# Optimization experiments

Hardware: AMD Instinct MI355X
Metric: run time of the kernel (lower is better)

## Reference

```python
import jax, jax.numpy as jnp
import numpy as np

B, H, W, D, C = 1, 32, 32, 32, 512
NH, P = 8, 8
HD = C // NH          # head dim = 64
N = P ** 3            # tokens per window = 512
HID = 4 * C           # mlp hidden = 2048
EPS = 1e-5            # torch LayerNorm default


def setup_inputs() -> dict:
    key = jax.random.key(0)
    ks = jax.random.split(key, 8)
    init = lambda k, shape, fan: jax.random.normal(k, shape, jnp.float32) / np.sqrt(fan).astype(np.float32)
    return {
        "x": jax.random.normal(ks[0], (B, H, W, D, C), jnp.float32),
        "q_ms": jax.random.normal(ks[1], (B, NH, N, HD), jnp.float32),
        "norm1_w": jnp.ones((C,), jnp.float32),
        "norm1_b": jnp.zeros((C,), jnp.float32),
        "kv_w": init(ks[2], (C, 2 * C), C),
        "kv_b": jnp.zeros((2 * C,), jnp.float32),
        "proj_w": init(ks[3], (C, C), C),
        "proj_b": jnp.zeros((C,), jnp.float32),
        "norm2_w": jnp.ones((C,), jnp.float32),
        "norm2_b": jnp.zeros((C,), jnp.float32),
        "fc1_w": init(ks[4], (C, HID), C),
        "fc1_b": jnp.zeros((HID,), jnp.float32),
        "fc2_w": init(ks[5], (HID, C), HID),
        "fc2_b": jnp.zeros((C,), jnp.float32),
    }


def layernorm(x, w, b):
    m = jnp.mean(x, axis=-1, keepdims=True)
    v = jnp.mean(jnp.square(x - m), axis=-1, keepdims=True)
    return (x - m) * jax.lax.rsqrt(v + EPS) * w + b


def reference(x, q_ms, norm1_w, norm1_b, kv_w, kv_b, proj_w, proj_b,
              norm2_w, norm2_b, fc1_w, fc1_b, fc2_w, fc2_b):
    shortcut = x
    xn = layernorm(x, norm1_w, norm1_b)
    # get_patches: (B,H,W,D,C) -> (B*nw, N, C), windows in (nh,nw,nd) order
    xw = xn.reshape(B, H // P, P, W // P, P, D // P, P, C)
    xw = xw.transpose(0, 1, 3, 5, 2, 4, 6, 7).reshape(-1, N, C)
    Bw = xw.shape[0]  # B * num_windows = 64
    # global attention: kv from window tokens, shared multi-scale query q_ms
    kv = (xw @ kv_w + kv_b).reshape(Bw, N, 2, NH, HD).transpose(2, 0, 3, 1, 4)
    k, v = kv[0], kv[1]  # (Bw, NH, N, HD)
    scale = HD ** -0.5
    q = jnp.tile(q_ms, (Bw // B, 1, 1, 1)) * scale  # replicate query across windows
    attn = jax.nn.softmax(jnp.einsum('bhqd,bhkd->bhqk', q, k), axis=-1)
    o = jnp.einsum('bhqk,bhkd->bhqd', attn, v)
    o = o.transpose(0, 2, 1, 3).reshape(Bw, N, C)
    o = o @ proj_w + proj_b
    # get_image: (B*nw, N, C) -> (B,H,W,D,C)
    xi = o.reshape(B, H // P, W // P, D // P, P, P, P, C)
    xi = xi.transpose(0, 1, 4, 2, 5, 3, 6, 7).reshape(B, H, W, D, C)
    x1 = shortcut + xi
    h = layernorm(x1, norm2_w, norm2_b)
    h = jax.nn.gelu(h @ fc1_w + fc1_b, approximate=False) @ fc2_w + fc2_b
    return x1 + h
```

## Files before the change

### kernel.cpp

```cpp
#include <hip/hip_runtime.h>

typedef unsigned short u16;
typedef __attribute__((ext_vector_type(8))) short bfrag;
typedef __attribute__((ext_vector_type(4))) float ffrag;

#define LN_EPS 1e-5f

#define GLOAD16(g, l)                                                          \
    __builtin_amdgcn_global_load_lds(                                          \
        (const __attribute__((address_space(1))) void*)(g),                    \
        (__attribute__((address_space(3))) void*)(l), 16, 0, 0)

__device__ __forceinline__ u16 f2bf(float f) {
    unsigned u = __builtin_bit_cast(unsigned, f);
    u += 0x7fffu + ((u >> 16) & 1u);
    return (u16)(u >> 16);
}

__device__ __forceinline__ int win_to_img(int tok) {
    int win = tok >> 9, n = tok & 511;
    int wh = win >> 4, ww = (win >> 2) & 3, wd = win & 3;
    int ph = n >> 6, pw = (n >> 3) & 7, pd = n & 7;
    return ((wh * 8 + ph) * 32 + (ww * 8 + pw)) * 32 + (wd * 8 + pd);
}

__global__ __launch_bounds__(256) void k_ln(const float* __restrict__ x,
                                            const float* __restrict__ w,
                                            const float* __restrict__ b,
                                            u16* __restrict__ out, int windowed) {
    int wave = threadIdx.x >> 6, lane = threadIdx.x & 63;
    int tok = blockIdx.x * 4 + wave;
    int src = windowed ? win_to_img(tok) : tok;
    const float* xr = x + (size_t)src * 512;
    float v[8];
#pragma unroll
    for (int i = 0; i < 2; i++) {
        float4 f = *(const float4*)(xr + i * 256 + lane * 4);
        v[i * 4 + 0] = f.x; v[i * 4 + 1] = f.y; v[i * 4 + 2] = f.z; v[i * 4 + 3] = f.w;
    }
    float s = 0.f;
#pragma unroll
    for (int i = 0; i < 8; i++) s += v[i];
#pragma unroll
    for (int m = 1; m < 64; m <<= 1) s += __shfl_xor(s, m);
    float mean = s * (1.0f / 512.0f);
    float vs = 0.f;
#pragma unroll
    for (int i = 0; i < 8; i++) { float d = v[i] - mean; vs += d * d; }
#pragma unroll
    for (int m = 1; m < 64; m <<= 1) vs += __shfl_xor(vs, m);
    float rstd = rsqrtf(vs * (1.0f / 512.0f) + LN_EPS);
    u16* orow = out + (size_t)tok * 512;
#pragma unroll
    for (int i = 0; i < 2; i++) {
        int c0 = i * 256 + lane * 4;
        ushort4 o;
        o.x = f2bf((v[i * 4 + 0] - mean) * rstd * w[c0 + 0] + b[c0 + 0]);
        o.y = f2bf((v[i * 4 + 1] - mean) * rstd * w[c0 + 1] + b[c0 + 1]);
        o.z = f2bf((v[i * 4 + 2] - mean) * rstd * w[c0 + 2] + b[c0 + 2]);
        o.w = f2bf((v[i * 4 + 3] - mean) * rstd * w[c0 + 3] + b[c0 + 3]);
        *(ushort4*)(orow + c0) = o;
    }
}

__global__ __launch_bounds__(256) void k_prep(const float* __restrict__ kv_w,
                                              const float* __restrict__ proj_w,
                                              const float* __restrict__ fc1_w,
                                              const float* __restrict__ fc2_w,
                                              const float* __restrict__ q,
                                              u16* __restrict__ kv_wt,
                                              u16* __restrict__ proj_wt,
                                              u16* __restrict__ fc1_wt,
                                              u16* __restrict__ fc2_wt,
                                              u16* __restrict__ qbf) {
    int i = blockIdx.x * 256 + threadIdx.x;
    if (i < 524288) {
        int n = i >> 9, k = i & 511;
        kv_wt[i] = f2bf(kv_w[k * 1024 + n]);
    } else if (i < 786432) {
        int j = i - 524288, n = j >> 9, k = j & 511;
        proj_wt[j] = f2bf(proj_w[k * 512 + n]);
    } else if (i < 1835008) {
        int j = i - 786432, n = j >> 9, k = j & 511;
        fc1_wt[j] = f2bf(fc1_w[k * 2048 + n]);
    } else if (i < 2883584) {
        int j = i - 1835008, n = j >> 11, k = j & 2047;
        fc2_wt[j] = f2bf(fc2_w[k * 512 + n]);
    } else {
        int j = i - 2883584;
        qbf[j] = f2bf(q[j] * 0.125f);
    }
}

template <int EPI>
__global__ __launch_bounds__(256, 4) void k_gemm128(const u16* __restrict__ A,
                                                    const u16* __restrict__ Bt,
                                                    const float* __restrict__ bias,
                                                    void* __restrict__ Cout, int K, int Nn,
                                                    const float* __restrict__ resid,
                                                    void* __restrict__ Cout2) {
    __shared__ u16 As0[4096], Bs0[4096], As1[4096], Bs1[4096];
    int tid = threadIdx.x;
    int wave = tid >> 6, lane = tid & 63;
    int wr = wave >> 1, wc = wave & 1;

    int gx = Nn >> 7;
    int nwg = gridDim.x;
    int wg = blockIdx.x;
    int wgs = (wg & 7) * (nwg >> 3) + (wg >> 3);
    int bn = wgs % gx, bm = wgs / gx;

    int rt = wave * 32 + (lane >> 2);
    int sxo = ((lane & 3) ^ ((rt ^ (rt >> 2)) & 3)) * 8;
    const u16* Ag = A + (size_t)(bm * 128 + rt) * K + sxo;
    const u16* Bg = Bt + (size_t)(bn * 128 + rt) * K + sxo;

    int fr = lane & 15, g = lane >> 4;
    int pco = (g ^ ((fr ^ (fr >> 2)) & 3)) * 8;

    ffrag acc[4][4] = {};

#define STAGE(AS, BS, k0)                                                      \
    {                                                                          \
        GLOAD16(Ag + (k0), AS + wave * 1024);                                  \
        GLOAD16(Ag + (k0) + 16 * K, AS + wave * 1024 + 512);                   \
        GLOAD16(Bg + (k0), BS + wave * 1024);                                  \
        GLOAD16(Bg + (k0) + 16 * K, BS + wave * 1024 + 512);                   \
    }
#define COMPUTE(AS, BS)                                                        \
    {                                                                          \
        bfrag a[4], b[4];                                                      \
        _Pragma("unroll") for (int m = 0; m < 4; m++)                          \
            a[m] = *(const bfrag*)(AS + (wr * 64 + m * 16 + fr) * 32 + pco);   \
        _Pragma("unroll") for (int n = 0; n < 4; n++)                          \
            b[n] = *(const bfrag*)(BS + (wc * 64 + n * 16 + fr) * 32 + pco);   \
        _Pragma("unroll") for (int m = 0; m < 4; m++)                          \
            _Pragma("unroll") for (int n = 0; n < 4; n++)                      \
                acc[m][n] = __builtin_amdgcn_mfma_f32_16x16x32_bf16(           \
                    a[m], b[n], acc[m][n], 0, 0, 0);                           \
    }

    int nt = K >> 5;
    STAGE(As0, Bs0, 0);
    __syncthreads();
    int t = 0;
    for (; t + 2 < nt; t += 2) {
        STAGE(As1, Bs1, (t + 1) * 32);
        COMPUTE(As0, Bs0);
        __syncthreads();
        STAGE(As0, Bs0, (t + 2) * 32);
        COMPUTE(As1, Bs1);
        __syncthreads();
    }
    STAGE(As1, Bs1, (nt - 1) * 32);
    COMPUTE(As0, Bs0);
    __syncthreads();
    COMPUTE(As1, Bs1);
#undef STAGE
#undef COMPUTE

    int gcolb = bn * 128 + wc * 64;
    int grb = bm * 128 + wr * 64;

    if constexpr (EPI == 0 || EPI == 2) {
        __syncthreads();
        u16* ep = (wave == 0) ? As0 : (wave == 1) ? Bs0 : (wave == 2) ? As1 : Bs1;
        int h = (gcolb >> 6) & 7;
        bool isK = (EPI == 2) || (gcolb < 512);
#pragma unroll
        for (int m = 0; m < 4; m++)
#pragma unroll
            for (int n = 0; n < 4; n++) {
                float bv = bias[gcolb + n * 16 + fr];
#pragma unroll
                for (int r = 0; r < 4; r++) {
                    int wq = m * 16 + g * 4 + r;
                    int wcc = n * 16 + fr;
                    float val = acc[m][n][r] + bv;
                    if constexpr (EPI == 2) {
                        float xx = val;
                        float inner = fmaf(0.044715f * xx * xx, xx, xx);
                        float e = __expf(-1.5957691216f * inner);
                        val = xx * __builtin_amdgcn_rcpf(1.0f + e);
                    }
                    if (isK)
                        ep[wq * 64 + (wcc ^ ((wq & 7) << 3))] = f2bf(val);
                    else
                        ep[wcc * 64 + (wq ^ ((wcc & 7) << 3))] = f2bf(val);
                }
            }
#pragma unroll
        for (int rd = 0; rd < 8; rd++) {
            int row = rd * 8 + (lane >> 3);
            int ch = (lane & 7) ^ (row & 7);
            int4 v = *(const int4*)(ep + row * 64 + ch * 8);
            if constexpr (EPI == 2) {
                int grow = grb + row;
                *(int4*)(&((u16*)Cout)[(size_t)grow * Nn + gcolb + (lane & 7) * 8]) = v;
            } else {
                if (isK) {
                    int tok = grb + row;
                    int win = tok >> 9, key = tok & 511;
                    *(int4*)(&((u16*)Cout)[(((size_t)(win * 8 + h)) * 512 + key) * 64 + (lane & 7) * 8]) = v;
                } else {
                    int win = grb >> 9, key0 = grb & 511;
                    *(int4*)(&((u16*)Cout2)[(((size_t)(win * 8 + h)) * 64 + row) * 512 + key0 + (lane & 7) * 8]) = v;
                }
            }
        }
    } else {
#pragma unroll
        for (int m = 0; m < 4; m++)
#pragma unroll
            for (int n = 0; n < 4; n++) {
                int col = gcolb + n * 16 + fr;
                float bv = bias[col];
#pragma unroll
                for (int r = 0; r < 4; r++) {
                    int row = grb + m * 16 + g * 4 + r;
                    float val = acc[m][n][r] + bv;
                    if constexpr (EPI == 1) {
                        int ri = win_to_img(row);
                        size_t o = (size_t)ri * 512 + col;
                        ((float*)Cout)[o] = val + resid[o];
                    } else {
                        size_t o = (size_t)row * 512 + col;
                        ((float*)Cout)[o] = val + resid[o];
                    }
                }
            }
    }
}

__global__ __launch_bounds__(256, 4) void k_attn(const u16* __restrict__ qb,
                                                 const u16* __restrict__ kb,
                                                 const u16* __restrict__ vtb,
                                                 u16* __restrict__ o) {
    __shared__ u16 K0[4096], K1[4096], V0[4096], V1[4096];
    __shared__ u16 Ps[4096];
    int bid = blockIdx.x;
    int wg = (bid & 7) * 512 + (bid >> 3);
    int qc = wg & 7;
    int pair = wg >> 3;
    int hh = pair & 7, win = pair >> 3;
    int wave = threadIdx.x >> 6, lane = threadIdx.x & 63;
    const u16* kbw = kb + ((size_t)(win * 8 + hh)) * 512 * 64;
    const u16* vtw = vtb + ((size_t)(win * 8 + hh)) * 64 * 512;

    const u16* qrow = qb + ((size_t)hh * 512 + qc * 64 + (wave << 4) + (lane & 15)) * 64 + (lane >> 4) * 8;
    bfrag aq0 = *(const bfrag*)(qrow);
    bfrag aq1 = *(const bfrag*)(qrow + 32);

    ffrag acc[4] = {};
    float m_run[4], l_run[4];
#pragma unroll
    for (int r = 0; r < 4; r++) { m_run[r] = -1e30f; l_run[r] = 0.0f; }

    int srow = lane >> 3;
    int sxo = ((lane & 7) ^ srow) * 8;
    int fr = lane & 15;
    int fkc = lane >> 4;
    int kx0 = (fkc ^ (fr & 7)) * 8;
    int kx1 = ((fkc + 4) ^ (fr & 7)) * 8;
    int arow = (wave << 4) + fr;
    int pswz = (arow & 7) << 3;

#define STAGE_KV(KS, VS, kc)                                                   \
    {                                                                          \
        GLOAD16(kbw + (size_t)((kc) * 64 + wave * 8 + srow) * 64 + sxo,        \
                KS + wave * 512);                                              \
        GLOAD16(kbw + (size_t)((kc) * 64 + 32 + wave * 8 + srow) * 64 + sxo,   \
                KS + 2048 + wave * 512);                                       \
        GLOAD16(vtw + (size_t)(wave * 8 + srow) * 512 + (kc) * 64 + sxo,       \
                VS + wave * 512);                                              \
        GLOAD16(vtw + (size_t)(32 + wave * 8 + srow) * 512 + (kc) * 64 + sxo,  \
                VS + 2048 + wave * 512);                                       \
    }
#define ATT_COMPUTE(KS, VS)                                                    \
    {                                                                          \
        ffrag s[4] = {};                                                       \
        _Pragma("unroll") for (int j = 0; j < 4; j++) {                        \
            bfrag b0 = *(const bfrag*)(KS + (j * 16 + fr) * 64 + kx0);         \
            s[j] = __builtin_amdgcn_mfma_f32_16x16x32_bf16(aq0, b0, s[j], 0, 0, 0); \
            bfrag b1 = *(const bfrag*)(KS + (j * 16 + fr) * 64 + kx1);         \
            s[j] = __builtin_amdgcn_mfma_f32_16x16x32_bf16(aq1, b1, s[j], 0, 0, 0); \
        }                                                                      \
        int need = 0;                                                          \
        _Pragma("unroll") for (int r = 0; r < 4; r++) {                        \
            float mxj = fmaxf(fmaxf(s[0][r], s[1][r]),                         \
                              fmaxf(s[2][r], s[3][r]));                        \
            need |= (mxj > m_run[r] + 8.0f) ? 1 : 0;                           \
        }                                                                      \
        if (__any(need)) {                                                     \
            _Pragma("unroll") for (int r = 0; r < 4; r++) {                    \
                float mx = fmaxf(fmaxf(s[0][r], s[1][r]),                      \
                                 fmaxf(s[2][r], s[3][r]));                     \
                _Pragma("unroll") for (int d = 1; d < 16; d <<= 1)             \
                    mx = fmaxf(mx, __shfl_xor(mx, d));                         \
                float mnew = fmaxf(m_run[r], mx);                              \
                float alpha = __expf(m_run[r] - mnew);                         \
                m_run[r] = mnew;                                               \
                l_run[r] *= alpha;                                             \
                _Pragma("unroll") for (int j = 0; j < 4; j++)                  \
                    acc[j][r] *= alpha;                                        \
            }                                                                  \
        }                                                                      \
        _Pragma("unroll") for (int j = 0; j < 4; j++)                          \
            _Pragma("unroll") for (int r = 0; r < 4; r++) {                    \
                float p = __expf(s[j][r] - m_run[r]);                          \
                l_run[r] += p;                                                 \
                int prow = (wave << 4) + (lane >> 4) * 4 + r;                  \
                Ps[prow * 64 + ((j * 16 + fr) ^ ((prow & 7) << 3))] = f2bf(p); \
            }                                                                  \
        bfrag ap0 = *(const bfrag*)(&Ps[arow * 64 + ((fkc * 8) ^ pswz)]);      \
        bfrag ap1 = *(const bfrag*)(&Ps[arow * 64 + ((32 + fkc * 8) ^ pswz)]); \
        _Pragma("unroll") for (int j = 0; j < 4; j++) {                        \
            bfrag v0 = *(const bfrag*)(VS + (j * 16 + fr) * 64 + kx0);         \
            acc[j] = __builtin_amdgcn_mfma_f32_16x16x32_bf16(ap0, v0, acc[j], 0, 0, 0); \
            bfrag v1 = *(const bfrag*)(VS + (j * 16 + fr) * 64 + kx1);         \
            acc[j] = __builtin_amdgcn_mfma_f32_16x16x32_bf16(ap1, v1, acc[j], 0, 0, 0); \
        }                                                                      \
    }

    STAGE_KV(K0, V0, 0);
    __syncthreads();
#pragma unroll 1
    for (int kc = 0; kc < 8; kc += 2) {
        if (kc + 1 < 8) STAGE_KV(K1, V1, kc + 1);
        ATT_COMPUTE(K0, V0);
        __syncthreads();
        if (kc + 2 < 8) STAGE_KV(K0, V0, kc + 2);
        ATT_COMPUTE(K1, V1);
        __syncthreads();
    }
#undef STAGE_KV
#undef ATT_COMPUTE

#pragma unroll
    for (int r = 0; r < 4; r++) {
#pragma unroll
        for (int d = 1; d < 16; d <<= 1)
            l_run[r] += __shfl_xor(l_run[r], d);
    }

    int row0 = qc * 64 + (wave << 4) + (lane >> 4) * 4;
#pragma unroll
    for (int j = 0; j < 4; j++) {
        int col = hh * 64 + j * 16 + fr;
#pragma unroll
        for (int r = 0; r < 4; r++) {
            float val = acc[j][r] / l_run[r];
            o[((size_t)win * 512 + row0 + r) * 512 + col] = f2bf(val);
        }
    }
}

extern "C" void kernel_launch(void* const* d_in, const int* in_sizes, int n_in,
                              void* d_out, int out_size, void* d_ws, size_t ws_size,
                              hipStream_t stream) {
    const float* x      = (const float*)d_in[0];
    const float* q_ms   = (const float*)d_in[1];
    const float* n1w    = (const float*)d_in[2];
    const float* n1b    = (const float*)d_in[3];
    const float* kv_w   = (const float*)d_in[4];
    const float* kv_b   = (const float*)d_in[5];
    const float* proj_w = (const float*)d_in[6];
    const float* proj_b = (const float*)d_in[7];
    const float* n2w    = (const float*)d_in[8];
    const float* n2b    = (const float*)d_in[9];
    const float* fc1_w  = (const float*)d_in[10];
    const float* fc1_b  = (const float*)d_in[11];
    const float* fc2_w  = (const float*)d_in[12];
    const float* fc2_b  = (const float*)d_in[13];

    char* ws = (char*)d_ws;
    const size_t OFF_XNW = 0;
    const size_t OFF_KB  = 33554432;
    const size_t OFF_VT  = 67108864;
    const size_t OFF_O   = 100663296;
    const size_t OFF_HID = 0;
    const size_t OFF_X1  = 134217728;
    const size_t OFF_XN2 = 201326592;
    const size_t OFF_W   = 234881024;
    u16* xnw = (u16*)(ws + OFF_XNW);
    u16* kbb = (u16*)(ws + OFF_KB);
    u16* vtb = (u16*)(ws + OFF_VT);
    u16* ob  = (u16*)(ws + OFF_O);
    u16* hid = (u16*)(ws + OFF_HID);
    float* x1 = (float*)(ws + OFF_X1);
    u16* xn2 = (u16*)(ws + OFF_XN2);
    u16* kv_wt   = (u16*)(ws + OFF_W);
    u16* proj_wt = kv_wt + 512 * 1024;
    u16* fc1_wt  = proj_wt + 512 * 512;
    u16* fc2_wt  = fc1_wt + 512 * 2048;
    u16* qbf     = fc2_wt + 2048 * 512;
    size_t need = OFF_W + (size_t)(512 * 1024 + 512 * 512 + 512 * 2048 + 2048 * 512 + 8 * 512 * 64) * 2;
    if (ws_size < need) return;

    k_ln<<<8192, 256, 0, stream>>>(x, n1w, n1b, xnw, 1);
    k_prep<<<12288, 256, 0, stream>>>(kv_w, proj_w, fc1_w, fc2_w, q_ms,
                                      kv_wt, proj_wt, fc1_wt, fc2_wt, qbf);

    k_gemm128<0><<<2048, 256, 0, stream>>>(xnw, kv_wt, kv_b, kbb, 512, 1024, nullptr, vtb);
    k_attn<<<dim3(4096), 256, 0, stream>>>(qbf, kbb, vtb, ob);
    k_gemm128<1><<<1024, 256, 0, stream>>>(ob, proj_wt, proj_b, x1, 512, 512, x, nullptr);
    k_ln<<<8192, 256, 0, stream>>>(x1, n2w, n2b, xn2, 0);
    k_gemm128<2><<<4096, 256, 0, stream>>>(xn2, fc1_wt, fc1_b, hid, 512, 2048, nullptr, nullptr);
    k_gemm128<3><<<1024, 256, 0, stream>>>(hid, fc2_wt, fc2_b, d_out, 2048, 512, x1, nullptr);
}
```

Measured before the change: 437.9 us.

## Use 256x256-tile 512-thread GEMM kernel for MLP fc1 and fc2

```diff
diff --git a/kernel.cpp b/kernel.cpp
--- a/kernel.cpp
+++ b/kernel.cpp
@@ -162,11 +162,11 @@
     int gcolb = bn * 128 + wc * 64;
     int grb = bm * 128 + wr * 64;
 
-    if constexpr (EPI == 0 || EPI == 2) {
+    if constexpr (EPI == 0) {
         __syncthreads();
         u16* ep = (wave == 0) ? As0 : (wave == 1) ? Bs0 : (wave == 2) ? As1 : Bs1;
         int h = (gcolb >> 6) & 7;
-        bool isK = (EPI == 2) || (gcolb < 512);
+        bool isK = (gcolb < 512);
 #pragma unroll
         for (int m = 0; m < 4; m++)
 #pragma unroll
@@ -177,12 +177,6 @@
                     int wq = m * 16 + g * 4 + r;
                     int wcc = n * 16 + fr;
                     float val = acc[m][n][r] + bv;
-                    if constexpr (EPI == 2) {
-                        float xx = val;
-                        float inner = fmaf(0.044715f * xx * xx, xx, xx);
-                        float e = __expf(-1.5957691216f * inner);
-                        val = xx * __builtin_amdgcn_rcpf(1.0f + e);
-                    }
                     if (isK)
                         ep[wq * 64 + (wcc ^ ((wq & 7) << 3))] = f2bf(val);
                     else
@@ -194,18 +188,13 @@
             int row = rd * 8 + (lane >> 3);
             int ch = (lane & 7) ^ (row & 7);
             int4 v = *(const int4*)(ep + row * 64 + ch * 8);
-            if constexpr (EPI == 2) {
-                int grow = grb + row;
-                *(int4*)(&((u16*)Cout)[(size_t)grow * Nn + gcolb + (lane & 7) * 8]) = v;
+            if (isK) {
+                int tok = grb + row;
+                int win = tok >> 9, key = tok & 511;
+                *(int4*)(&((u16*)Cout)[(((size_t)(win * 8 + h)) * 512 + key) * 64 + (lane & 7) * 8]) = v;
             } else {
-                if (isK) {
-                    int tok = grb + row;
-                    int win = tok >> 9, key = tok & 511;
-                    *(int4*)(&((u16*)Cout)[(((size_t)(win * 8 + h)) * 512 + key) * 64 + (lane & 7) * 8]) = v;
-                } else {
-                    int win = grb >> 9, key0 = grb & 511;
-                    *(int4*)(&((u16*)Cout2)[(((size_t)(win * 8 + h)) * 64 + row) * 512 + key0 + (lane & 7) * 8]) = v;
-                }
+                int win = grb >> 9, key0 = grb & 511;
+                *(int4*)(&((u16*)Cout2)[(((size_t)(win * 8 + h)) * 64 + row) * 512 + key0 + (lane & 7) * 8]) = v;
             }
         }
     } else {
@@ -219,14 +208,141 @@
                 for (int r = 0; r < 4; r++) {
                     int row = grb + m * 16 + g * 4 + r;
                     float val = acc[m][n][r] + bv;
-                    if constexpr (EPI == 1) {
-                        int ri = win_to_img(row);
-                        size_t o = (size_t)ri * 512 + col;
-                        ((float*)Cout)[o] = val + resid[o];
-                    } else {
-                        size_t o = (size_t)row * 512 + col;
-                        ((float*)Cout)[o] = val + resid[o];
-                    }
+                    int ri = win_to_img(row);
+                    size_t o = (size_t)ri * 512 + col;
+                    ((float*)Cout)[o] = val + resid[o];
+                }
+            }
+    }
+}
+
+template <int EPI>
+__global__ __launch_bounds__(512, 2) void k_gemm256p(const u16* __restrict__ A,
+                                                     const u16* __restrict__ Bt,
+                                                     const float* __restrict__ bias,
+                                                     void* __restrict__ Cout, int K, int Nn,
+                                                     const float* __restrict__ resid) {
+    __shared__ u16 sm[65536];
+    int tid = threadIdx.x;
+    int wave = tid >> 6, lane = tid & 63;
+    int wm = wave >> 2, wn = wave & 3;
+
+    int gx = Nn >> 8;
+    int nwg = gridDim.x;
+    int wg = blockIdx.x;
+    int wgs = (wg & 7) * (nwg >> 3) + (wg >> 3);
+    int bn = wgs % gx, bm = wgs / gx;
+
+    int sr = tid >> 3;
+    int sf = (sr ^ (sr >> 2)) & 7;
+    int sxo = ((tid & 7) ^ sf) * 8;
+    const u16* Ag = A + (size_t)(bm * 256 + sr) * K + sxo;
+    const u16* Bg = Bt + (size_t)(bn * 256 + sr) * K + sxo;
+    size_t rowK = (size_t)64 * K;
+
+    int fr = lane & 15, g = lane >> 4;
+    int fb0 = (fr ^ (fr >> 2)) & 7;
+
+    ffrag acc[8][4] = {};
+
+#define STAGE256(SLOT, k0)                                                     \
+    {                                                                          \
+        u16* d = sm + (SLOT) * 32768 + wave * 512;                             \
+        _Pragma("unroll") for (int i = 0; i < 4; i++)                          \
+            GLOAD16(Ag + (k0) + i * rowK, d + i * 4096);                       \
+        _Pragma("unroll") for (int i = 0; i < 4; i++)                          \
+            GLOAD16(Bg + (k0) + i * rowK, d + 16384 + i * 4096);               \
+    }
+
+    int nt = K >> 6;
+    STAGE256(0, 0);
+    asm volatile("s_waitcnt vmcnt(0)" ::: "memory");
+    __builtin_amdgcn_sched_barrier(0);
+    __builtin_amdgcn_s_barrier();
+    __builtin_amdgcn_sched_barrier(0);
+
+#pragma unroll 1
+    for (int t = 0; t < nt; ++t) {
+        const u16* Ab = sm + (t & 1) * 32768;
+        const u16* Bb = Ab + 16384;
+        if (t + 1 < nt) STAGE256((t + 1) & 1, (size_t)(t + 1) * 64);
+        bfrag bfr[8];
+#pragma unroll
+        for (int n = 0; n < 4; n++)
+#pragma unroll
+            for (int s = 0; s < 2; s++)
+                bfr[n * 2 + s] = *(const bfrag*)(Bb + (wn * 64 + n * 16 + fr) * 64 +
+                                  (((g + 4 * s) ^ fb0 ^ ((n & 1) << 2)) & 7) * 8);
+#pragma unroll
+        for (int q = 0; q < 4; q++) {
+            bfrag afr[4];
+#pragma unroll
+            for (int mm = 0; mm < 2; mm++)
+#pragma unroll
+                for (int s = 0; s < 2; s++) {
+                    int m = q * 2 + mm;
+                    afr[mm * 2 + s] = *(const bfrag*)(Ab + (wm * 128 + m * 16 + fr) * 64 +
+                                      (((g + 4 * s) ^ fb0 ^ ((m & 1) << 2)) & 7) * 8);
+                }
+            __builtin_amdgcn_s_setprio(1);
+#pragma unroll
+            for (int mm = 0; mm < 2; mm++)
+#pragma unroll
+                for (int n = 0; n < 4; n++)
+#pragma unroll
+                    for (int s = 0; s < 2; s++)
+                        acc[q * 2 + mm][n] = __builtin_amdgcn_mfma_f32_16x16x32_bf16(
+                            afr[mm * 2 + s], bfr[n * 2 + s], acc[q * 2 + mm][n], 0, 0, 0);
+            __builtin_amdgcn_s_setprio(0);
+        }
+        asm volatile("s_waitcnt lgkmcnt(0)" ::: "memory");
+        asm volatile("s_waitcnt vmcnt(0)" ::: "memory");
+        __builtin_amdgcn_sched_barrier(0);
+        __builtin_amdgcn_s_barrier();
+        __builtin_amdgcn_sched_barrier(0);
+    }
+#undef STAGE256
+
+    int gcb = bn * 256 + wn * 64;
+    int grb = bm * 256 + wm * 128;
+
+    if constexpr (EPI == 2) {
+        u16* ep = sm + wave * 8192;
+#pragma unroll
+        for (int m = 0; m < 8; m++)
+#pragma unroll
+            for (int n = 0; n < 4; n++) {
+                float bv = bias[gcb + n * 16 + fr];
+#pragma unroll
+                for (int r = 0; r < 4; r++) {
+                    int rl = m * 16 + g * 4 + r;
+                    int cl = n * 16 + fr;
+                    float xx = acc[m][n][r] + bv;
+                    float inner = fmaf(0.044715f * xx * xx, xx, xx);
+                    float e = __expf(-1.5957691216f * inner);
+                    float val = xx * __builtin_amdgcn_rcpf(1.0f + e);
+                    ep[rl * 64 + (cl ^ ((rl & 7) << 3))] = f2bf(val);
+                }
+            }
+#pragma unroll
+        for (int it = 0; it < 16; it++) {
+            int rl = it * 8 + (lane >> 3);
+            int ch = (lane & 7) ^ (rl & 7);
+            int4 v = *(const int4*)(ep + rl * 64 + ch * 8);
+            *(int4*)(&((u16*)Cout)[(size_t)(grb + rl) * Nn + gcb + (lane & 7) * 8]) = v;
+        }
+    } else {
+#pragma unroll
+        for (int m = 0; m < 8; m++)
+#pragma unroll
+            for (int n = 0; n < 4; n++) {
+                int col = gcb + n * 16 + fr;
+                float bv = bias[col];
+#pragma unroll
+                for (int r = 0; r < 4; r++) {
+                    int row = grb + m * 16 + g * 4 + r;
+                    size_t o = (size_t)row * 512 + col;
+                    ((float*)Cout)[o] = acc[m][n][r] + bv + resid[o];
                 }
             }
     }
@@ -405,6 +521,6 @@
     k_attn<<<dim3(4096), 256, 0, stream>>>(qbf, kbb, vtb, ob);
     k_gemm128<1><<<1024, 256, 0, stream>>>(ob, proj_wt, proj_b, x1, 512, 512, x, nullptr);
     k_ln<<<8192, 256, 0, stream>>>(x1, n2w, n2b, xn2, 0);
-    k_gemm128<2><<<4096, 256, 0, stream>>>(xn2, fc1_wt, fc1_b, hid, 512, 2048, nullptr, nullptr);
-    k_gemm128<3><<<1024, 256, 0, stream>>>(hid, fc2_wt, fc2_b, d_out, 2048, 512, x1, nullptr);
-}
+    k_gemm256p<2><<<1024, 512, 0, stream>>>(xn2, fc1_wt, fc1_b, hid, 512, 2048, nullptr);
+    k_gemm256p<3><<<256, 512, 0, stream>>>(hid, fc2_wt, fc2_b, d_out, 2048, 512, x1);
+}
```

New measurement: 413.7 us. 1.06x faster.
